# Performance work log

Measured on AMD Instinct MI355X. Metric: run time of the kernel, lower is better.

The kernel has to match this reference:

```python
import jax, jax.numpy as jnp
import numpy as np

B, N, M, C, T, HF, WF = 4, 512, 32, 512, 8, 14, 14
K = 80          # num_classes
P = 7           # ROI pool output size
HID = 1024
IMG = 224


def setup_inputs() -> dict:
    key = jax.random.key(0)
    k0, k1, k2, k3, k4, k5 = jax.random.split(key, 6)
    feature = jax.random.normal(k0, (B, C, T, HF, WF), dtype=jnp.float32)
    # GT boxes: realistic xyxy boxes inside a 224x224 image
    ka, kb = jax.random.split(k1)
    cxy = jax.random.uniform(ka, (B, M, 2), minval=40.0, maxval=180.0)
    wh = jax.random.uniform(kb, (B, M, 2), minval=40.0, maxval=100.0)
    gt_bboxes = jnp.concatenate([cxy - wh / 2, cxy + wh / 2], axis=-1).astype(jnp.float32)
    # Proposals: jittered copies of GT boxes so many pass the IoU>=0.85 fg test
    idx = jnp.arange(N) % M
    base = gt_bboxes[:, idx]                                   # [B,N,4]
    noise = jax.random.normal(k2, (B, N, 4), dtype=jnp.float32) * 1.5
    proposal_bboxes = jnp.clip(base + noise, 0.0, float(IMG))
    gt_classes = (jax.random.uniform(k3, (B, M, K)) < 0.1).astype(jnp.float32)
    W1 = jax.random.normal(k4, (C * P * P, HID), dtype=jnp.float32) * 0.01
    b1 = jnp.zeros((HID,), jnp.float32)
    W2 = jax.random.normal(k5, (HID, K), dtype=jnp.float32) * 0.01
    b2 = jnp.zeros((K,), jnp.float32)
    return {"feature": feature, "proposal_bboxes": proposal_bboxes,
            "gt_bboxes": gt_bboxes, "gt_classes": gt_classes,
            "W1": W1, "b1": b1, "W2": W2, "b2": b2,
            "image_h": IMG, "image_w": IMG}


def _iou(a, b):
    # a [B,N,4], b [B,M,4] xyxy -> [B,N,M]
    lt = jnp.maximum(a[:, :, None, :2], b[:, None, :, :2])
    rb = jnp.minimum(a[:, :, None, 2:], b[:, None, :, 2:])
    wh = jnp.clip(rb - lt, 0.0)
    inter = wh[..., 0] * wh[..., 1]
    area_a = (a[..., 2] - a[..., 0]) * (a[..., 3] - a[..., 1])
    area_b = (b[..., 2] - b[..., 0]) * (b[..., 3] - b[..., 1])
    return inter / (area_a[:, :, None] + area_b[:, None, :] - inter + 1e-8)


def _roi_pool(feat_bhwc, boxes, bidx, sy, sx):
    # feat_bhwc [B,H,W,C]; boxes [R,4] image coords; bilinear 7x7 ROI pooling
    H, W = feat_bhwc.shape[1], feat_bhwc.shape[2]
    x1, y1, x2, y2 = boxes[:, 0] * sx, boxes[:, 1] * sy, boxes[:, 2] * sx, boxes[:, 3] * sy
    g = (jnp.arange(P, dtype=jnp.float32) + 0.5) / P
    ys = y1[:, None] + g[None, :] * (y2 - y1)[:, None]        # [R,P]
    xs = x1[:, None] + g[None, :] * (x2 - x1)[:, None]        # [R,P]
    y = jnp.broadcast_to(ys[:, :, None], (boxes.shape[0], P, P)) - 0.5
    x = jnp.broadcast_to(xs[:, None, :], (boxes.shape[0], P, P)) - 0.5
    y0f = jnp.floor(y); x0f = jnp.floor(x)
    wy = jnp.clip(y - y0f, 0.0, 1.0)[..., None]
    wx = jnp.clip(x - x0f, 0.0, 1.0)[..., None]
    y0 = jnp.clip(y0f, 0, H - 1).astype(jnp.int32)
    y1i = jnp.clip(y0f + 1, 0, H - 1).astype(jnp.int32)
    x0 = jnp.clip(x0f, 0, W - 1).astype(jnp.int32)
    x1i = jnp.clip(x0f + 1, 0, W - 1).astype(jnp.int32)
    bi = bidx[:, None, None]
    gather = lambda yy, xx: feat_bhwc[bi, yy, xx]             # [R,P,P,C]
    out = (gather(y0, x0) * (1 - wy) * (1 - wx) + gather(y0, x1i) * (1 - wy) * wx +
           gather(y1i, x0) * wy * (1 - wx) + gather(y1i, x1i) * wy * wx)
    return out


def reference(feature, proposal_bboxes, gt_bboxes, gt_classes, W1, b1, W2, b2, image_h, image_w):
    # temporal average pool (AvgPool3d over T) -> [B,C,HF,WF]
    feat = feature.mean(axis=2)
    feat_bhwc = jnp.transpose(feat, (0, 2, 3, 1))             # [B,HF,WF,C]
    # IoU-based fg assignment
    ious = _iou(proposal_bboxes, gt_bboxes)                   # [B,N,M]
    max_iou = ious.max(axis=2)                                # [B,N]
    assign = ious.argmax(axis=2)                              # [B,N]
    any_fg = jnp.any(max_iou >= 0.85)
    thresh = jnp.where(any_fg, 0.85, 0.5)                     # fallback branch
    fg = (max_iou >= thresh).astype(feature.dtype)            # [B,N]
    # ROI pool all proposals (bg masked out in the loss)
    boxes = proposal_bboxes.reshape(B * N, 4)
    bidx = jnp.repeat(jnp.arange(B, dtype=jnp.int32), N)
    sy = feat.shape[2] / float(image_h)
    sx = feat.shape[3] / float(image_w)
    pool = _roi_pool(feat_bhwc, boxes, bidx, sy, sx)          # [R,P,P,C]
    pool = jnp.transpose(pool, (0, 3, 1, 2)).reshape(B * N, C * P * P)
    hidden = jax.nn.relu(pool @ W1 + b1)                      # [R,HID]
    logits = hidden @ W2 + b2                                 # [R,K]
    # multilabel soft-margin labels per proposal
    labels = gt_classes[jnp.repeat(jnp.arange(B), N), assign.reshape(-1)]  # [R,K]
    per = -(labels * jax.nn.log_sigmoid(logits) +
            (1.0 - labels) * jax.nn.log_sigmoid(-logits)).mean(axis=-1)    # [R]
    per = per.reshape(B, N)
    cnt = fg.sum(axis=1)
    losses = jnp.where(cnt > 0, (per * fg).sum(axis=1) / jnp.maximum(cnt, 1.0), 0.0)
    return losses
```

## Files before the change

### kernel.cpp

```cpp
#include <hip/hip_runtime.h>
#include <cstdint>
#include <cstddef>

#define KTOT 25088
#define NBOX 2048
#define HID  1024

typedef __bf16 bf16x8 __attribute__((ext_vector_type(8)));
typedef float  f32x4  __attribute__((ext_vector_type(4)));

__device__ __forceinline__ unsigned short f2bf(float f) {
  union { float f; unsigned u; } v; v.f = f;
  unsigned r = v.u + 0x7FFFu + ((v.u >> 16) & 1u);
  return (unsigned short)(r >> 16);
}

__device__ __forceinline__ float scalar_f(const void* p) {
  int iv = *(const int*)p;
  if (iv > 0 && iv < (1 << 20)) return (float)iv;
  return *(const float*)p;
}

__global__ __launch_bounds__(256) void k_meant(const float* __restrict__ feature,
                                               float* __restrict__ fbhwc) {
  int id = blockIdx.x * 256 + threadIdx.x;
  if (id >= 4 * 512 * 196) return;
  int pix = id % 196;
  int c   = (id / 196) & 511;
  int b   = id / (196 * 512);
  const float* p = feature + ((size_t)(b * 512 + c) * 8) * 196 + pix;
  float s = 0.f;
#pragma unroll
  for (int t = 0; t < 8; ++t) s += p[t * 196];
  fbhwc[((size_t)(b * 196 + pix)) * 512 + c] = s * 0.125f;
}

__global__ __launch_bounds__(256) void k_iou(const float* __restrict__ prop,
                                             const float* __restrict__ gtb,
                                             float* __restrict__ max_iou,
                                             int* __restrict__ assign,
                                             int* __restrict__ flag) {
  __shared__ float g[128];
  int gid = blockIdx.x * 256 + threadIdx.x;
  int b = gid >> 9;
  if (threadIdx.x < 128) g[threadIdx.x] = gtb[b * 128 + threadIdx.x];
  __syncthreads();
  float x1 = prop[gid * 4 + 0], y1 = prop[gid * 4 + 1];
  float x2 = prop[gid * 4 + 2], y2 = prop[gid * 4 + 3];
  float aa = (x2 - x1) * (y2 - y1);
  float best = -1e30f; int arg = 0;
  for (int m = 0; m < 32; ++m) {
    float gx1 = g[m*4], gy1 = g[m*4+1], gx2 = g[m*4+2], gy2 = g[m*4+3];
    float iw = fmaxf(fminf(x2, gx2) - fmaxf(x1, gx1), 0.f);
    float ih = fmaxf(fminf(y2, gy2) - fmaxf(y1, gy1), 0.f);
    float inter = iw * ih;
    float ab = (gx2 - gx1) * (gy2 - gy1);
    float iou = inter / (aa + ab - inter + 1e-8f);
    if (iou > best) { best = iou; arg = m; }
  }
  max_iou[gid] = best; assign[gid] = arg;
  if (best >= 0.85f) atomicOr(flag, 1);
}

__global__ __launch_bounds__(256) void k_w1t(const float* __restrict__ W1,
                                             unsigned short* __restrict__ W1T) {
  __shared__ unsigned short tile[64][68];
  int kp0 = blockIdx.x * 64;
  int h0  = blockIdx.y * 64;
  int t = threadIdx.x;
  int seg = t & 15, ro = t >> 4;
#pragma unroll
  for (int r = 0; r < 4; ++r) {
    int i = ro + r * 16;
    int kp = kp0 + i;
    int srow = (kp & 511) * 49 + (kp >> 9);
    float4 v = *(const float4*)(W1 + (size_t)srow * 1024 + h0 + seg * 4);
    tile[i][seg*4+0] = f2bf(v.x);
    tile[i][seg*4+1] = f2bf(v.y);
    tile[i][seg*4+2] = f2bf(v.z);
    tile[i][seg*4+3] = f2bf(v.w);
  }
  __syncthreads();
#pragma unroll
  for (int r = 0; r < 4; ++r) {
    int hi = ro + r * 16;
    unsigned a = tile[seg*4+0][hi];
    unsigned b = tile[seg*4+1][hi];
    unsigned c = tile[seg*4+2][hi];
    unsigned d = tile[seg*4+3][hi];
    *(uint2*)(W1T + (size_t)(h0+hi)*KTOT + kp0 + seg*4) =
        make_uint2(a | (b << 16), c | (d << 16));
  }
}

__global__ __launch_bounds__(256) void k_roipool(const float* __restrict__ fbhwc,
                                                 const float* __restrict__ prop,
                                                 const void* ihp, const void* iwp,
                                                 unsigned short* __restrict__ Apool) {
  int n = blockIdx.x;
  int tid = threadIdx.x;
  float sy = 14.f / scalar_f(ihp);
  float sx = 14.f / scalar_f(iwp);
  float bx1 = prop[n*4+0]*sx, by1 = prop[n*4+1]*sy;
  float bx2 = prop[n*4+2]*sx, by2 = prop[n*4+3]*sy;
  const float* fb = fbhwc + (size_t)(n >> 9) * 196 * 512;
  unsigned short* arow = Apool + (size_t)n * KTOT;
  int c4 = (tid & 127) << 2;
  int bh = tid >> 7;
  for (int b2i = 0; b2i < 49; b2i += 2) {
    int bin = b2i + bh;
    if (bin >= 49) continue;
    int py = bin / 7, px = bin - py * 7;
    float y = by1 + ((py + 0.5f) * (1.f/7.f)) * (by2 - by1) - 0.5f;
    float x = bx1 + ((px + 0.5f) * (1.f/7.f)) * (bx2 - bx1) - 0.5f;
    float y0f = floorf(y), x0f = floorf(x);
    float wy = y - y0f, wx = x - x0f;
    int y0  = min(max((int)y0f, 0), 13);
    int y1i = min(max((int)y0f + 1, 0), 13);
    int x0  = min(max((int)x0f, 0), 13);
    int x1i = min(max((int)x0f + 1, 0), 13);
    float w00 = (1.f - wy) * (1.f - wx), w01 = (1.f - wy) * wx;
    float w10 = wy * (1.f - wx),         w11 = wy * wx;
    const float4 f00 = *(const float4*)(fb + (y0 * 14 + x0 ) * 512 + c4);
    const float4 f01 = *(const float4*)(fb + (y0 * 14 + x1i) * 512 + c4);
    const float4 f10 = *(const float4*)(fb + (y1i * 14 + x0 ) * 512 + c4);
    const float4 f11 = *(const float4*)(fb + (y1i * 14 + x1i) * 512 + c4);
    float vx = f00.x*w00 + f01.x*w01 + f10.x*w10 + f11.x*w11;
    float vy = f00.y*w00 + f01.y*w01 + f10.y*w10 + f11.y*w11;
    float vz = f00.z*w00 + f01.z*w01 + f10.z*w10 + f11.z*w11;
    float vw = f00.w*w00 + f01.w*w01 + f10.w*w10 + f11.w*w11;
    unsigned lo = (unsigned)f2bf(vx) | ((unsigned)f2bf(vy) << 16);
    unsigned hi = (unsigned)f2bf(vz) | ((unsigned)f2bf(vw) << 16);
    *(uint2*)(arow + bin * 512 + c4) = make_uint2(lo, hi);
  }
}

__device__ __forceinline__ void gload16(const unsigned short* g, unsigned short* l) {
  __builtin_amdgcn_global_load_lds(
      (const __attribute__((address_space(1))) unsigned int*)g,
      (__attribute__((address_space(3))) unsigned int*)l, 16, 0, 0);
}

__global__ __launch_bounds__(512, 2) void k_gemm1(
    const unsigned short* __restrict__ A,
    const unsigned short* __restrict__ B,
    unsigned short* __restrict__ hp)
{
  extern __shared__ unsigned short lds[];
  const int tid  = threadIdx.x;
  const int w    = tid >> 6;
  const int lane = tid & 63;
  const int wr = w >> 2, wc = w & 3;
  const int bid = (int)blockIdx.x;
  const int wg  = (bid & 7) * 32 + (bid >> 3);
  const int kb  = wg >> 5;
  const int gy  = (wg >> 2) & 7;
  const int gx  = wg & 3;

  f32x4 acc[8][4];
  const f32x4 zero = {0.f, 0.f, 0.f, 0.f};
#pragma unroll
  for (int m = 0; m < 8; ++m)
#pragma unroll
    for (int n = 0; n < 4; ++n) acc[m][n] = zero;

  const int row0 = tid >> 2;
  const int qdst = tid & 3;
  const int qsrc = qdst ^ ((tid >> 3) & 3);
  const int ldA0 = row0 * 32 + qdst * 8;
  const int ldA1 = ldA0 + 4096;
  const size_t kbase = (size_t)kb * 3136;
  const unsigned short* gA0 = A + (size_t)(gy * 256 + row0) * KTOT + kbase + qsrc * 8;
  const unsigned short* gA1 = gA0 + (size_t)128 * KTOT;
  const unsigned short* gB0 = B + (size_t)(gx * 256 + row0) * KTOT + kbase + qsrc * 8;
  const unsigned short* gB1 = gB0 + (size_t)128 * KTOT;

  const int l15 = lane & 15;
  const int qsw = ((lane >> 4) ^ ((l15 >> 1) & 3)) * 8;
  int aoff[8], boff[4];
#pragma unroll
  for (int m = 0; m < 8; ++m) aoff[m] = (wr * 128 + m * 16 + l15) * 32 + qsw;
#pragma unroll
  for (int n = 0; n < 4; ++n) boff[n] = (wc * 64 + n * 16 + l15) * 32 + qsw;

#pragma unroll
  for (int t = 0; t < 4; ++t) {
    unsigned short* Ab = lds + t * 8192;
    unsigned short* Bb = lds + 32768 + t * 8192;
    gload16(gA0 + t * 32, Ab + ldA0);
    gload16(gA1 + t * 32, Ab + ldA1);
    gload16(gB0 + t * 32, Bb + ldA0);
    gload16(gB1 + t * 32, Bb + ldA1);
  }
  int cur = 0;

#define GTILE(VM, DOSTAGE, KNEXT) do {                                        \
    asm volatile("s_waitcnt vmcnt(" #VM ")" ::: "memory");                    \
    __builtin_amdgcn_s_barrier();                                             \
    const unsigned short* Ab = lds + cur * 8192;                              \
    const unsigned short* Bb = lds + 32768 + cur * 8192;                      \
    bf16x8 af[8], bfr[4];                                                     \
    _Pragma("unroll") for (int m = 0; m < 8; ++m)                             \
      af[m] = *reinterpret_cast<const bf16x8*>(Ab + aoff[m]);                 \
    _Pragma("unroll") for (int n = 0; n < 4; ++n)                             \
      bfr[n] = *reinterpret_cast<const bf16x8*>(Bb + boff[n]);                \
    asm volatile("s_waitcnt lgkmcnt(0)" ::: "memory");                        \
    __builtin_amdgcn_s_barrier();                                             \
    __builtin_amdgcn_sched_barrier(0);                                        \
    if (DOSTAGE) {                                                            \
      const size_t go = (size_t)(KNEXT) * 32;                                 \
      unsigned short* An = lds + cur * 8192;                                  \
      unsigned short* Bn = lds + 32768 + cur * 8192;                          \
      gload16(gA0 + go, An + ldA0);                                           \
      gload16(gA1 + go, An + ldA1);                                           \
      gload16(gB0 + go, Bn + ldA0);                                           \
      gload16(gB1 + go, Bn + ldA1);                                           \
    }                                                                         \
    __builtin_amdgcn_s_setprio(1);                                            \
    _Pragma("unroll") for (int m = 0; m < 8; ++m)                             \
      _Pragma("unroll") for (int n = 0; n < 4; ++n)                           \
        acc[m][n] = __builtin_amdgcn_mfma_f32_16x16x32_bf16(af[m], bfr[n],    \
                                                            acc[m][n], 0, 0, 0); \
    __builtin_amdgcn_s_setprio(0);                                            \
    cur = (cur + 1) & 3;                                                      \
  } while (0)

  for (int kk = 0; kk < 94; ++kk) { GTILE(12, true, kk + 4); }
  GTILE(12, false, 0);
  GTILE(8,  false, 0);
  GTILE(4,  false, 0);
  GTILE(0,  false, 0);
#undef GTILE

  unsigned short* o = hp + (size_t)kb * (2048u * 1024u);
  const int r0 = gy * 256 + wr * 128 + ((lane >> 4) << 2);
  const int c0 = gx * 256 + wc * 64 + l15;
#pragma unroll
  for (int m = 0; m < 8; ++m)
#pragma unroll
    for (int n = 0; n < 4; ++n)
#pragma unroll
      for (int j = 0; j < 4; ++j)
        o[(size_t)(r0 + m * 16 + j) * 1024 + c0 + n * 16] = f2bf(acc[m][n][j]);
}

template<int OUTBF>
__global__ __launch_bounds__(256, 4) void k_gemm(
    const unsigned short* __restrict__ A,
    const unsigned short* __restrict__ B,
    void* __restrict__ outp,
    int Kst, int kIters, int nTileBits, int mTileBits, int ldc)
{
  __shared__ unsigned short As[2][4096];
  __shared__ unsigned short Bs[2][4096];
  const int tid  = threadIdx.x;
  const int w    = tid >> 6;
  const int lane = tid & 63;
  const int nwg = (int)gridDim.x, cpx = nwg >> 3;
  const int bid = (int)blockIdx.x;
  const int wg  = (bid & 7) * cpx + (bid >> 3);
  const int kb  = wg >> (mTileBits + nTileBits);
  const int rem = wg & ((1 << (mTileBits + nTileBits)) - 1);
  const int gy  = rem >> nTileBits;
  const int gx  = rem & ((1 << nTileBits) - 1);
  const int wr = w >> 1, wc = w & 1;

  f32x4 acc[4][4];
  const f32x4 zero = {0.f, 0.f, 0.f, 0.f};
#pragma unroll
  for (int m = 0; m < 4; ++m)
#pragma unroll
    for (int n = 0; n < 4; ++n) acc[m][n] = zero;

  const int r0   = 32 * w + (lane >> 2);
  const int qsrc = (lane & 3) ^ ((lane >> 3) & 3);
  const size_t kbase = (size_t)kb * kIters * 32;
  const unsigned short* gA = A + (size_t)(gy * 128 + r0) * Kst + kbase + qsrc * 8;
  const unsigned short* gB = B + (size_t)(gx * 128 + r0) * Kst + kbase + qsrc * 8;
  const int ldst = r0 * 32 + (lane & 3) * 8;

  const int swq = ((lane >> 4) ^ ((lane >> 1) & 3)) * 8;
  const int ar = (wr * 64 + (lane & 15)) * 32 + swq;
  const int br = (wc * 64 + (lane & 15)) * 32 + swq;

#define STAGE(bufi, it) do {                                         \
    const unsigned short* pa = gA + (size_t)(it) * 32;               \
    const unsigned short* pb = gB + (size_t)(it) * 32;               \
    gload16(pa,                      &As[bufi][ldst]);               \
    gload16(pa + (size_t)16 * Kst,   &As[bufi][ldst + 512]);         \
    gload16(pb,                      &Bs[bufi][ldst]);               \
    gload16(pb + (size_t)16 * Kst,   &Bs[bufi][ldst + 512]);         \
  } while (0)

  STAGE(0, 0);
  int cur = 0;
  for (int kk = 0; kk < kIters; ++kk) {
    __syncthreads();
    if (kk + 1 < kIters) STAGE(cur ^ 1, kk + 1);
    bf16x8 af[4], bfr[4];
#pragma unroll
    for (int m = 0; m < 4; ++m)
      af[m] = *reinterpret_cast<const bf16x8*>(&As[cur][ar + m * 512]);
#pragma unroll
    for (int n = 0; n < 4; ++n)
      bfr[n] = *reinterpret_cast<const bf16x8*>(&Bs[cur][br + n * 512]);
#pragma unroll
    for (int m = 0; m < 4; ++m)
#pragma unroll
      for (int n = 0; n < 4; ++n)
        acc[m][n] = __builtin_amdgcn_mfma_f32_16x16x32_bf16(af[m], bfr[n], acc[m][n], 0, 0, 0);
    cur ^= 1;
  }
#undef STAGE

  const size_t M = (size_t)(1 << mTileBits) * 128;
  const size_t splitStride = M * (size_t)ldc;
  const int r0o = gy * 128 + wr * 64 + ((lane >> 4) << 2);
  const int c0o = gx * 128 + wc * 64 + (lane & 15);
  if (OUTBF) {
    unsigned short* o = (unsigned short*)outp + (size_t)kb * splitStride;
#pragma unroll
    for (int m = 0; m < 4; ++m)
#pragma unroll
      for (int n = 0; n < 4; ++n)
#pragma unroll
        for (int j = 0; j < 4; ++j)
          o[(size_t)(r0o + m * 16 + j) * ldc + c0o + n * 16] = f2bf(acc[m][n][j]);
  } else {
    float* o = (float*)outp + (size_t)kb * splitStride;
#pragma unroll
    for (int m = 0; m < 4; ++m)
#pragma unroll
      for (int n = 0; n < 4; ++n)
#pragma unroll
        for (int j = 0; j < 4; ++j)
          o[(size_t)(r0o + m * 16 + j) * ldc + c0o + n * 16] = acc[m][n][j];
  }
}

__global__ __launch_bounds__(256) void k_combine(const unsigned short* __restrict__ hp,
                                                 const float* __restrict__ b1,
                                                 unsigned short* __restrict__ hidden) {
  int gid = blockIdx.x * 256 + threadIdx.x;
  int id8 = gid * 8;
  int h = id8 & 1023;
  float a[8];
#pragma unroll
  for (int j = 0; j < 8; ++j) a[j] = b1[h + j];
#pragma unroll
  for (int s = 0; s < 8; ++s) {
    uint4 u = *(const uint4*)(hp + (size_t)s * 2097152 + id8);
    unsigned uu[4] = {u.x, u.y, u.z, u.w};
#pragma unroll
    for (int q = 0; q < 4; ++q) {
      union { unsigned u; float f; } lo, hi;
      lo.u = uu[q] << 16; hi.u = uu[q] & 0xFFFF0000u;
      a[2*q]   += lo.f;
      a[2*q+1] += hi.f;
    }
  }
  unsigned out[4];
#pragma unroll
  for (int q = 0; q < 4; ++q) {
    unsigned l  = f2bf(fmaxf(a[2*q],   0.f));
    unsigned hh = f2bf(fmaxf(a[2*q+1], 0.f));
    out[q] = l | (hh << 16);
  }
  *(uint4*)(hidden + id8) = make_uint4(out[0], out[1], out[2], out[3]);
}

__global__ __launch_bounds__(256) void k_w2t(const float* __restrict__ W2,
                                             unsigned short* __restrict__ W2T) {
  int id = blockIdx.x * 256 + threadIdx.x;
  int cls = id >> 10, k = id & 1023;
  float v = (cls < 80) ? W2[(size_t)k * 80 + cls] : 0.f;
  W2T[id] = f2bf(v);
}

__global__ __launch_bounds__(256) void k_bce(const float* __restrict__ hp2,
                                             const float* __restrict__ b2,
                                             const float* __restrict__ gtc,
                                             const int* __restrict__ assign,
                                             float* __restrict__ per) {
  __shared__ float red[256];
  int t = threadIdx.x;
  int box = t >> 4, li = t & 15;
  int n = blockIdx.x * 16 + box;
  int lab = ((n >> 9) * 32 + assign[n]) * 80;
  float s = 0.f;
#pragma unroll
  for (int j = 0; j < 5; ++j) {
    int c = li + 16 * j;
    size_t o = (size_t)n * 128 + c;
    float x = hp2[o] + hp2[o + 262144] + hp2[o + 524288] + hp2[o + 786432] + b2[c];
    float y = gtc[lab + c];
    float ce = log1pf(expf(-fabsf(x)));
    s += y * (fmaxf(-x, 0.f) + ce) + (1.f - y) * (fmaxf(x, 0.f) + ce);
  }
  red[t] = s;
  __syncthreads();
  if (li == 0) {
    float tot = 0.f;
#pragma unroll
    for (int i = 0; i < 16; ++i) tot += red[box * 16 + i];
    per[n] = tot * (1.f / 80.f);
  }
}

__global__ __launch_bounds__(512) void k_reduce(const float* __restrict__ per,
                                                const float* __restrict__ max_iou,
                                                const int* __restrict__ flag,
                                                float* __restrict__ out) {
  __shared__ float sv[8], sf[8];
  int b = blockIdx.x, tid = threadIdx.x;
  float thr = (*flag) ? 0.85f : 0.5f;
  int n = b * 512 + tid;
  float f = (max_iou[n] >= thr) ? 1.f : 0.f;
  float v = per[n] * f;
#pragma unroll
  for (int o = 32; o > 0; o >>= 1) {
    v += __shfl_down(v, o);
    f += __shfl_down(f, o);
  }
  int wv = tid >> 6;
  if ((tid & 63) == 0) { sv[wv] = v; sf[wv] = f; }
  __syncthreads();
  if (tid == 0) {
    float S = 0.f, F = 0.f;
#pragma unroll
    for (int i = 0; i < 8; ++i) { S += sv[i]; F += sf[i]; }
    out[b] = (F > 0.f) ? S / fmaxf(F, 1.f) : 0.f;
  }
}

extern "C" void kernel_launch(void* const* d_in, const int* in_sizes, int n_in,
                              void* d_out, int out_size, void* d_ws, size_t ws_size,
                              hipStream_t stream) {
  const float* feature = (const float*)d_in[0];
  const float* prop    = (const float*)d_in[1];
  const float* gtb     = (const float*)d_in[2];
  const float* gtc     = (const float*)d_in[3];
  const float* W1      = (const float*)d_in[4];
  const float* b1      = (const float*)d_in[5];
  const float* W2      = (const float*)d_in[6];
  const float* b2      = (const float*)d_in[7];
  const void*  ihp     = d_in[8];
  const void*  iwp     = d_in[9];

  char* ws = (char*)d_ws;
  float*          fbhwc  = (float*)(ws);
  unsigned short* W1T    = (unsigned short*)(ws + 1605632);
  unsigned short* Apool  = (unsigned short*)(ws + 52985856);
  unsigned short* hp     = (unsigned short*)(ws + 155746304);
  float*          max_iou= (float*)(ws + 189300736);
  int*            assign = (int*)(ws + 189308928);
  float*          per    = (float*)(ws + 189317120);
  int*            flag   = (int*)(ws + 189325312);
  unsigned short* hidden = W1T;
  unsigned short* W2T    = Apool;
  float*          hp2    = (float*)((char*)Apool + 262144);

  hipFuncSetAttribute((const void*)k_gemm1,
                      hipFuncAttributeMaxDynamicSharedMemorySize, 131072);

  hipMemsetAsync(flag, 0, sizeof(int), stream);
  k_meant  <<<1568, 256, 0, stream>>>(feature, fbhwc);
  k_iou    <<<8, 256, 0, stream>>>(prop, gtb, max_iou, assign, flag);
  k_w1t    <<<dim3(392, 16), 256, 0, stream>>>(W1, W1T);
  k_roipool<<<2048, 256, 0, stream>>>(fbhwc, prop, ihp, iwp, Apool);
  k_gemm1  <<<256, 512, 131072, stream>>>(Apool, W1T, hp);
  k_combine<<<1024, 256, 0, stream>>>(hp, b1, hidden);
  k_w2t    <<<512, 256, 0, stream>>>(W2, W2T);
  k_gemm<0><<<64, 256, 0, stream>>>(hidden, W2T, hp2, 1024, 8, 0, 4, 128);
  k_bce    <<<128, 256, 0, stream>>>(hp2, b2, gtc, assign, per);
  k_reduce <<<4, 512, 0, stream>>>(per, max_iou, flag, (float*)d_out);
}
```

Baseline: 203.1 us.

## Restructure gemm1 main loop into 4-phase ping-pong with interleaved staging

Replaces the 4-deep single-tile pipeline in the split-K GEMM1 kernel with a two-buffer scheme that processes 64-wide K chunks in four phases. Each phase interleaves LDS fragment reads, global-to-LDS staging of the next chunk's A/B halves and a block of 16 MFMAs. It also switches to a new XOR swizzle for both the staging destination and the fragment read offsets. The aim is finer-grained overlap of memory and MFMA work and fewer bank conflicts, at the cost of more barriers per K step and a complex wait-count scheme that is easy to get wrong.

```diff
diff --git a/kernel.cpp b/kernel.cpp
--- a/kernel.cpp
+++ b/kernel.cpp
@@ -150,6 +150,7 @@
   const int tid  = threadIdx.x;
   const int w    = tid >> 6;
   const int lane = tid & 63;
+  const int l15  = lane & 15;
   const int wr = w >> 2, wc = w & 3;
   const int bid = (int)blockIdx.x;
   const int wg  = (bid & 7) * 32 + (bid >> 3);
@@ -164,73 +165,90 @@
 #pragma unroll
     for (int n = 0; n < 4; ++n) acc[m][n] = zero;
 
-  const int row0 = tid >> 2;
-  const int qdst = tid & 3;
-  const int qsrc = qdst ^ ((tid >> 3) & 3);
-  const int ldA0 = row0 * 32 + qdst * 8;
-  const int ldA1 = ldA0 + 4096;
+  const int xsw  = (tid & 7) ^ ((tid >> 3) & 7);
+  const int rloc = ((tid >> 3) << 1) + (xsw >> 2);
+  const int qsrc = xsw & 3;
   const size_t kbase = (size_t)kb * 3136;
-  const unsigned short* gA0 = A + (size_t)(gy * 256 + row0) * KTOT + kbase + qsrc * 8;
-  const unsigned short* gA1 = gA0 + (size_t)128 * KTOT;
-  const unsigned short* gB0 = B + (size_t)(gx * 256 + row0) * KTOT + kbase + qsrc * 8;
-  const unsigned short* gB1 = gB0 + (size_t)128 * KTOT;
-
-  const int l15 = lane & 15;
-  const int qsw = ((lane >> 4) ^ ((l15 >> 1) & 3)) * 8;
-  int aoff[8], boff[4];
-#pragma unroll
-  for (int m = 0; m < 8; ++m) aoff[m] = (wr * 128 + m * 16 + l15) * 32 + qsw;
-#pragma unroll
-  for (int n = 0; n < 4; ++n) boff[n] = (wc * 64 + n * 16 + l15) * 32 + qsw;
-
-#pragma unroll
-  for (int t = 0; t < 4; ++t) {
-    unsigned short* Ab = lds + t * 8192;
-    unsigned short* Bb = lds + 32768 + t * 8192;
-    gload16(gA0 + t * 32, Ab + ldA0);
-    gload16(gA1 + t * 32, Ab + ldA1);
-    gload16(gB0 + t * 32, Bb + ldA0);
-    gload16(gB1 + t * 32, Bb + ldA1);
-  }
-  int cur = 0;
-
-#define GTILE(VM, DOSTAGE, KNEXT) do {                                        \
-    asm volatile("s_waitcnt vmcnt(" #VM ")" ::: "memory");                    \
-    __builtin_amdgcn_s_barrier();                                             \
-    const unsigned short* Ab = lds + cur * 8192;                              \
-    const unsigned short* Bb = lds + 32768 + cur * 8192;                      \
-    bf16x8 af[8], bfr[4];                                                     \
-    _Pragma("unroll") for (int m = 0; m < 8; ++m)                             \
-      af[m] = *reinterpret_cast<const bf16x8*>(Ab + aoff[m]);                 \
-    _Pragma("unroll") for (int n = 0; n < 4; ++n)                             \
-      bfr[n] = *reinterpret_cast<const bf16x8*>(Bb + boff[n]);                \
-    asm volatile("s_waitcnt lgkmcnt(0)" ::: "memory");                        \
-    __builtin_amdgcn_s_barrier();                                             \
-    __builtin_amdgcn_sched_barrier(0);                                        \
-    if (DOSTAGE) {                                                            \
-      const size_t go = (size_t)(KNEXT) * 32;                                 \
-      unsigned short* An = lds + cur * 8192;                                  \
-      unsigned short* Bn = lds + 32768 + cur * 8192;                          \
-      gload16(gA0 + go, An + ldA0);                                           \
-      gload16(gA1 + go, An + ldA1);                                           \
-      gload16(gB0 + go, Bn + ldA0);                                           \
-      gload16(gB1 + go, Bn + ldA1);                                           \
-    }                                                                         \
-    __builtin_amdgcn_s_setprio(1);                                            \
-    _Pragma("unroll") for (int m = 0; m < 8; ++m)                             \
-      _Pragma("unroll") for (int n = 0; n < 4; ++n)                           \
-        acc[m][n] = __builtin_amdgcn_mfma_f32_16x16x32_bf16(af[m], bfr[n],    \
-                                                            acc[m][n], 0, 0, 0); \
-    __builtin_amdgcn_s_setprio(0);                                            \
-    cur = (cur + 1) & 3;                                                      \
-  } while (0)
-
-  for (int kk = 0; kk < 94; ++kk) { GTILE(12, true, kk + 4); }
-  GTILE(12, false, 0);
-  GTILE(8,  false, 0);
-  GTILE(4,  false, 0);
-  GTILE(0,  false, 0);
-#undef GTILE
+  const unsigned short* gAp = A + (size_t)(gy * 256 + rloc) * KTOT + kbase + qsrc * 8;
+  const unsigned short* gBp = B + (size_t)(gx * 256 + rloc) * KTOT + kbase + qsrc * 8;
+  const int dstc = tid * 8;
+
+  const int pfr   = ((lane >> 4) | ((l15 & 1) << 2)) ^ (l15 >> 1);
+  const int aoffc = wr * 4096 + (l15 >> 1) * 64 + pfr * 8;
+  const int boffc = wc * 2048 + (l15 >> 1) * 64 + pfr * 8;
+
+  bf16x8 af[8], b0[2], b1[2];
+
+#define VMW2 asm volatile("s_waitcnt vmcnt(2)" ::: "memory");
+#define VMW0 asm volatile("s_waitcnt vmcnt(0)" ::: "memory");
+#define DSR_A(CB, UOFF) _Pragma("unroll") for (int m = 0; m < 8; ++m) \
+    af[m] = *reinterpret_cast<const bf16x8*>(lds + (CB) + (UOFF) + aoffc + m * 512);
+#define DSR_B(BV, CB, UOFF, NH) _Pragma("unroll") for (int nn = 0; nn < 2; ++nn) \
+    BV[nn] = *reinterpret_cast<const bf16x8*>(lds + (CB) + (UOFF) + boffc + ((NH)*2+nn) * 512);
+#define MM16(BV, NH) _Pragma("unroll") for (int m = 0; m < 8; ++m) \
+    _Pragma("unroll") for (int nn = 0; nn < 2; ++nn) \
+      acc[m][(NH)*2+nn] = __builtin_amdgcn_mfma_f32_16x16x32_bf16(af[m], BV[nn], acc[m][(NH)*2+nn], 0, 0, 0);
+#define STG(OB, UOFF, GP, KOFF) { \
+    gload16((GP) + (KOFF),                      lds + (OB) + (UOFF) + dstc); \
+    gload16((GP) + (KOFF) + (size_t)128 * KTOT, lds + (OB) + (UOFF) + 4096 + dstc); }
+#define PHTAIL \
+    __builtin_amdgcn_sched_barrier(0); \
+    __builtin_amdgcn_s_barrier(); \
+    asm volatile("s_waitcnt lgkmcnt(0)" ::: "memory"); \
+    __builtin_amdgcn_sched_barrier(0); \
+    __builtin_amdgcn_s_setprio(1);
+#define PHEND \
+    __builtin_amdgcn_s_setprio(0); \
+    __builtin_amdgcn_s_barrier();
+
+#define KSTEP(CB, OB, KN, DOST, VM1C)                                          \
+  {                                   \
+    DSR_A(CB, 0)                                                               \
+    DSR_B(b0, CB, 16384, 0)                                                    \
+    if (DOST) STG(OB, 0, gAp, KN)                                              \
+    PHTAIL  MM16(b0, 0)  PHEND                                                 \
+                                          \
+    VM1C                                                                       \
+    DSR_B(b1, CB, 16384, 1)                                                    \
+    if (DOST) STG(OB, 16384, gBp, KN)                                          \
+    PHTAIL  MM16(b1, 1)  PHEND                                                 \
+                                      \
+    DSR_A(CB, 8192)                                                            \
+    DSR_B(b0, CB, 24576, 0)                                                    \
+    if (DOST) STG(OB, 8192, gAp, (KN) + 32)                                    \
+    PHTAIL  MM16(b0, 0)  PHEND                                                 \
+                                          \
+    if (DOST) VMW2                                                             \
+    DSR_B(b1, CB, 24576, 1)                                                    \
+    if (DOST) STG(OB, 24576, gBp, (KN) + 32)                                   \
+    PHTAIL  MM16(b1, 1)  PHEND                                                 \
+  }
+
+  STG(0, 0,     gAp, 0)
+  STG(0, 16384, gBp, 0)
+  STG(0, 8192,  gAp, 32)
+  STG(0, 24576, gBp, 32)
+  asm volatile("s_waitcnt vmcnt(4)" ::: "memory");
+  __builtin_amdgcn_s_barrier();
+
+#pragma unroll 1
+  for (int s = 0; s < 48; s += 2) {
+    const int kn1 = (s + 1) * 64;
+    const int kn2 = (s + 2) * 64;
+    KSTEP(0,     32768, kn1, true, VMW2)
+    KSTEP(32768, 0,     kn2, true, VMW2)
+  }
+  KSTEP(0, 32768, 0, false, VMW0)
+
+#undef KSTEP
+#undef PHEND
+#undef PHTAIL
+#undef STG
+#undef MM16
+#undef DSR_B
+#undef DSR_A
+#undef VMW0
+#undef VMW2
 
   unsigned short* o = hp + (size_t)kb * (2048u * 1024u);
   const int r0 = gy * 256 + wr * 128 + ((lane >> 4) << 2);
```

Result: faster. 196.9 us (-3.0%).
